# Kernel tuning notes

Hardware: AMD Instinct MI355X
Metric: run time of the kernel (lower is better)

## Reference

```python
import jax, jax.numpy as jnp
import numpy as np

N = 100_000   # nodes
E = 1_600_000 # edges (avg degree 16)
D = 128       # feature dim (input = hidden = output = mlp hidden)
L = 3         # GIN layers
EPS = 0.0     # init_eps, not learned


def setup_inputs() -> dict:
    key = jax.random.key(0)
    ks = jax.random.split(key, 7)
    feat = jax.random.normal(ks[0], (N, D), jnp.float32)
    # scale weights ~ 1/sqrt(fan_in) for numerically sane activations
    W1 = jax.random.normal(ks[1], (L, D, D), jnp.float32) / np.float32(np.sqrt(D))
    b1 = jax.random.normal(ks[2], (L, D), jnp.float32) * 0.01
    W2 = jax.random.normal(ks[3], (L, D, D), jnp.float32) / np.float32(np.sqrt(D))
    b2 = jax.random.normal(ks[4], (L, D), jnp.float32) * 0.01
    src = jax.random.randint(ks[5], (E,), 0, N, dtype=jnp.int32)
    dst = jax.random.randint(ks[6], (E,), 0, N, dtype=jnp.int32)
    return {"feat": feat, "W1": W1, "b1": b1, "W2": W2, "b2": b2,
            "src": src, "dst": dst}


def reference(feat, W1, b1, W2, b2, src, dst):
    h = feat
    for i in range(L):
        # sum-aggregate neighbor (source) features into destination nodes
        neigh = jax.ops.segment_sum(h[src], dst, num_segments=N)  # [N, D]
        rst = (1.0 + EPS) * h + neigh
        # 2-layer MLP: hidden layer uses act+norm(none), last layer is plain linear
        if i < L - 1:
            h1 = jax.nn.relu(rst @ W1[i] + b1[i])
            h2 = h1 @ W2[i] + b2[i]
            h = jax.nn.relu(h2)  # ApplyNodeFunc: norm(none) -> relu
        else:
            # last GIN layer: activation 'none' everywhere
            h1 = rst @ W1[i] + b1[i]
            h = h1 @ W2[i] + b2[i]
    return h
```

## Files before the change

### kernel.cpp

```cpp
#include <hip/hip_runtime.h>
#include <hip/hip_bf16.h>

#define D 128
#define NBUCK_SHIFT 9
#define PAD_SLACK 2048

typedef __bf16 bf16x8 __attribute__((ext_vector_type(8)));
typedef float f32x4 __attribute__((ext_vector_type(4)));
typedef float f32x2 __attribute__((ext_vector_type(2)));
typedef int i32x4 __attribute__((ext_vector_type(4)));
typedef int i32x2 __attribute__((ext_vector_type(2)));
typedef unsigned int u32x4 __attribute__((ext_vector_type(4)));
typedef unsigned short u16x4_t __attribute__((ext_vector_type(4)));
typedef unsigned short u16x8_t __attribute__((ext_vector_type(8)));

__device__ __forceinline__ unsigned short f2b(float f) {
    __hip_bfloat16 h = __float2bfloat16(f);
    return __builtin_bit_cast(unsigned short, h);
}

__device__ __forceinline__ void acc8(f32x2* acc, u32x4 x) {
#pragma unroll
    for (int r = 0; r < 4; ++r) {
        f32x2 t;
        t[0] = __builtin_bit_cast(float, x[r] << 16);
        t[1] = __builtin_bit_cast(float, x[r] & 0xffff0000u);
        acc[r] += t;
    }
}

__global__ __launch_bounds__(256) void coarse_hist_kernel(
        const int* __restrict__ dst, int* __restrict__ bco, int E, int nbuck) {
    __shared__ int s[256];
    int t = threadIdx.x;
    s[t] = 0;
    __syncthreads();
    for (int i = blockIdx.x * 256 + t; i < E; i += gridDim.x * 256)
        atomicAdd(&s[dst[i] >> NBUCK_SHIFT], 1);
    __syncthreads();
    if (t < nbuck && s[t] > 0) atomicAdd(&bco[t], s[t]);
}

__global__ __launch_bounds__(256) void bucket_scan_kernel(
        const int* __restrict__ bco, int* __restrict__ bbase, int nbuck, int E) {
    __shared__ int s[256];
    int t = threadIdx.x;
    int c = (t < nbuck) ? bco[t] : 0;
    s[t] = c;
    __syncthreads();
    for (int o = 1; o < 256; o <<= 1) {
        int y = (t >= o) ? s[t - o] : 0;
        __syncthreads();
        s[t] += y;
        __syncthreads();
    }
    if (t < nbuck) bbase[t] = s[t] - c;
    if (t == 0) bbase[nbuck] = E;
}

__global__ __launch_bounds__(256) void bucket_kernel(
        const int* __restrict__ src, const int* __restrict__ dst,
        const int* __restrict__ bbase, int* __restrict__ bcursor,
        unsigned int* __restrict__ pairs, int E, int nbuck) {
    __shared__ int lcnt[256];
    __shared__ int lbase[256];
    int t = threadIdx.x;
    int base = blockIdx.x * 4096;
    if (t < nbuck) lcnt[t] = 0;
    __syncthreads();
    int d[16], s[16];
#pragma unroll
    for (int k = 0; k < 16; ++k) {
        int i = base + t + k * 256;
        if (i < E) {
            d[k] = dst[i];
            s[k] = src[i];
            atomicAdd(&lcnt[d[k] >> NBUCK_SHIFT], 1);
        } else {
            d[k] = -1;
            s[k] = 0;
        }
    }
    __syncthreads();
    if (t < nbuck) {
        int c = lcnt[t];
        int g = (c > 0) ? atomicAdd(&bcursor[t], c) : 0;
        lbase[t] = bbase[t] + g;
        lcnt[t] = 0;
    }
    __syncthreads();
#pragma unroll
    for (int k = 0; k < 16; ++k) {
        if (d[k] >= 0) {
            int b = d[k] >> NBUCK_SHIFT;
            int r = atomicAdd(&lcnt[b], 1);
            pairs[lbase[b] + r] = ((unsigned)s[k] << 9) | ((unsigned)d[k] & 511u);
        }
    }
}

__global__ __launch_bounds__(1024) void bucket_build_kernel(
        const unsigned int* __restrict__ pairs, const int* __restrict__ bbase,
        i32x2* __restrict__ rowse, int* __restrict__ col, int* __restrict__ rowhead,
        int N, int E) {
    __shared__ int cnt[512];
    __shared__ int off[512];
    int t = threadIdx.x;
    int b = blockIdx.x;
    int s0 = bbase[b], s1 = bbase[b + 1];
    int p0 = ((s0 + 3) & ~3) + b * PAD_SLACK;
    if (t < 512) cnt[t] = 0;
    __syncthreads();
    for (int i = s0 + t; i < s1; i += 1024)
        atomicAdd(&cnt[pairs[i] & 511u], 1);
    __syncthreads();
    int deg = (t < 512) ? cnt[t] : 0;
    int ovp = (deg > 15) ? ((deg - 15 + 3) & ~3) : 0;
    if (t < 512) off[t] = ovp;
    __syncthreads();
    for (int o = 1; o < 512; o <<= 1) {
        int y = (t < 512 && t >= o) ? off[t - o] : 0;
        __syncthreads();
        if (t < 512) off[t] += y;
        __syncthreads();
    }
    int v0 = b << NBUCK_SHIFT;
    int zoff = N << 8;
    if (t < 512) {
        int ex = off[t] - ovp;
        off[t] = ex;
        cnt[t] = 0;
        int v = v0 + t;
        if (v < N) {
            i32x2 se;
            se[0] = p0 + ex;
            se[1] = p0 + ex + ovp;
            rowse[v] = se;
            int* rhv = rowhead + (size_t)v * 16;
            rhv[0] = v << 8;
            int ninl = deg < 15 ? deg : 15;
            for (int q = 1 + ninl; q < 16; ++q) rhv[q] = zoff;
        }
    }
    __syncthreads();
    for (int i = s0 + t; i < s1; i += 1024) {
        unsigned int p = pairs[i];
        int li = (int)(p & 511u);
        int x = (int)(p >> 9);
        int s = atomicAdd(&cnt[li], 1);
        if (s < 15) rowhead[(size_t)(v0 + li) * 16 + 1 + s] = x << 8;
        else        col[p0 + off[li] + (s - 15)] = x << 8;
    }
    __syncthreads();
    if (t < 512) {
        int cc = cnt[t];
        int ovreal = (cc > 15) ? cc - 15 : 0;
        int base2 = p0 + off[t];
        int endp = base2 + ((ovreal + 3) & ~3);
        for (int q = base2 + ovreal; q < endp; ++q) col[q] = zoff;
    }
}

__global__ void f32_to_bf16_kernel(const float4* __restrict__ in, ushort4* __restrict__ out, int n4) {
    int i = blockIdx.x * blockDim.x + threadIdx.x;
    if (i < n4) {
        float4 f = in[i];
        ushort4 o;
        o.x = f2b(f.x); o.y = f2b(f.y); o.z = f2b(f.z); o.w = f2b(f.w);
        out[i] = o;
    }
}

__global__ void wtrans_kernel(const float* __restrict__ W1, const float* __restrict__ W2,
                              unsigned short* __restrict__ W1L, unsigned short* __restrict__ W2L,
                              int total) {
    int i = blockIdx.x * blockDim.x + threadIdx.x;
    if (i < total) {
        int l = i >> 14;
        int rem = i & 16383;
        int k = rem >> 7;
        int n = rem & 127;
        int nt = n >> 4, l15 = n & 15;
        int kb = k >> 5, lg = (k >> 3) & 3, j = k & 7;
        int o = ((l * 32 + nt * 4 + kb) * 64 + lg * 16 + l15) * 8 + j;
        W1L[o] = f2b(W1[i]);
        W2L[o] = f2b(W2[i]);
    }
}

#define RSTRIDE 136
__global__ __launch_bounds__(256, 4) void fused_kernel(
        const unsigned short* __restrict__ h, const i32x2* __restrict__ rowse,
        const int* __restrict__ col, const i32x4* __restrict__ rowhead,
        const unsigned short* __restrict__ W1L, const unsigned short* __restrict__ W2L,
        const float* __restrict__ b1, const float* __restrict__ b2,
        unsigned short* __restrict__ hOut, float* __restrict__ fOut,
        int mode, int ntiles, int N) {
    __shared__ float b1s[128], b2s[128];
    __shared__ unsigned short rstile[16 * RSTRIDE];
    __shared__ unsigned short h1buf[2560];
    int tid = threadIdx.x;
    if (tid < 128) b1s[tid] = b1[tid];
    else b2s[tid - 128] = b2[tid - 128];
    int wave = tid >> 6, lane = tid & 63;
    int v0 = blockIdx.x << 4;

    {
        int i = lane & 15;
        int j = lane >> 4;
        const char* __restrict__ hb = (const char*)h;
        unsigned ioff = (unsigned)i * 16u;
        for (int q = 0; q < 4; ++q) {
            int m = wave * 4 + q;
            int v = v0 + m;
            f32x2 accA[4], accB[4], accC[4], accD[4];
#pragma unroll
            for (int r = 0; r < 4; ++r) {
                accA[r] = (f32x2){0.f, 0.f};
                accB[r] = (f32x2){0.f, 0.f};
                accC[r] = (f32x2){0.f, 0.f};
                accD[r] = (f32x2){0.f, 0.f};
            }
            if (v < N) {
                i32x4 c4 = __builtin_nontemporal_load(&rowhead[(size_t)v * 4 + j]);
                i32x2 se = __builtin_nontemporal_load(&rowse[v]);
                u32x4 x0 = *(const u32x4*)(hb + ((unsigned)c4[0] + ioff));
                u32x4 x1 = *(const u32x4*)(hb + ((unsigned)c4[1] + ioff));
                u32x4 x2 = *(const u32x4*)(hb + ((unsigned)c4[2] + ioff));
                u32x4 x3 = *(const u32x4*)(hb + ((unsigned)c4[3] + ioff));
                int e = se[0] + 4 * j;
                int e1 = se[1];
                bool have = (e < e1);
                i32x4 o4;
                if (have) o4 = __builtin_nontemporal_load((const i32x4*)(col + e));
                acc8(accA, x0);
                acc8(accB, x1);
                acc8(accC, x2);
                acc8(accD, x3);
                while (have) {
                    int en = e + 16;
                    bool haven = (en < e1);
                    i32x4 o4n;
                    if (haven) o4n = __builtin_nontemporal_load((const i32x4*)(col + en));
                    u32x4 y0 = *(const u32x4*)(hb + ((unsigned)o4[0] + ioff));
                    u32x4 y1 = *(const u32x4*)(hb + ((unsigned)o4[1] + ioff));
                    u32x4 y2 = *(const u32x4*)(hb + ((unsigned)o4[2] + ioff));
                    u32x4 y3 = *(const u32x4*)(hb + ((unsigned)o4[3] + ioff));
                    acc8(accA, y0);
                    acc8(accB, y1);
                    acc8(accC, y2);
                    acc8(accD, y3);
                    o4 = o4n;
                    e = en;
                    have = haven;
                }
            }
            unsigned short outv[8];
#pragma unroll
            for (int r = 0; r < 4; ++r) {
                f32x2 s = (accA[r] + accB[r]) + (accC[r] + accD[r]);
                float lo = s[0], hi = s[1];
                lo += __shfl_xor(lo, 16);
                lo += __shfl_xor(lo, 32);
                hi += __shfl_xor(hi, 16);
                hi += __shfl_xor(hi, 32);
                outv[2 * r] = f2b(lo);
                outv[2 * r + 1] = f2b(hi);
            }
            if (j == 0) {
                u16x8_t o;
#pragma unroll
                for (int r = 0; r < 8; ++r) o[r] = outv[r];
                *(u16x8_t*)(rstile + m * RSTRIDE + i * 8) = o;
            }
        }
    }
    __syncthreads();

    int l15 = lane & 15, lg = lane >> 4;
    bf16x8 bfrag[4];
#pragma unroll
    for (int kb = 0; kb < 4; ++kb)
        bfrag[kb] = *(const bf16x8*)(rstile + l15 * RSTRIDE + lg * 8 + kb * 32);

    f32x4 acc[2];
#pragma unroll
    for (int t = 0; t < 2; ++t) acc[t] = (f32x4){0.f, 0.f, 0.f, 0.f};
#pragma unroll
    for (int kb = 0; kb < 4; ++kb)
#pragma unroll
        for (int t = 0; t < 2; ++t) {
            int nt = wave * 2 + t;
            bf16x8 wf = *(const bf16x8*)(W1L + ((nt * 4 + kb) * 64 + lane) * 8);
            acc[t] = __builtin_amdgcn_mfma_f32_16x16x32_bf16(wf, bfrag[kb], acc[t], 0, 0, 0);
        }
#pragma unroll
    for (int t = 0; t < 2; ++t) {
        int nt = wave * 2 + t;
        f32x4 bias = *(const f32x4*)(b1s + nt * 16 + lg * 4);
        int kb2 = nt >> 1;
        int lgk = (nt & 1) * 2 + (lg >> 1);
        int U = kb2 * 80 + l15 * 5 + lgk;
        u16x4_t o;
#pragma unroll
        for (int r = 0; r < 4; ++r) {
            float x = acc[t][r] + bias[r];
            if (mode == 0) x = fmaxf(x, 0.f);
            o[r] = f2b(x);
        }
        *(u16x4_t*)(h1buf + U * 8 + (lg & 1) * 4) = o;
    }
    __syncthreads();
    bf16x8 bf2[4];
#pragma unroll
    for (int kb = 0; kb < 4; ++kb)
        bf2[kb] = *(const bf16x8*)(h1buf + (kb * 80 + l15 * 5 + lg) * 8);
#pragma unroll
    for (int t = 0; t < 2; ++t) acc[t] = (f32x4){0.f, 0.f, 0.f, 0.f};
#pragma unroll
    for (int kb = 0; kb < 4; ++kb)
#pragma unroll
        for (int t = 0; t < 2; ++t) {
            int nt = wave * 2 + t;
            bf16x8 wf = *(const bf16x8*)(W2L + ((nt * 4 + kb) * 64 + lane) * 8);
            acc[t] = __builtin_amdgcn_mfma_f32_16x16x32_bf16(wf, bf2[kb], acc[t], 0, 0, 0);
        }
    int m = v0 + l15;
    if (m < N) {
#pragma unroll
        for (int t = 0; t < 2; ++t) {
            int nt = wave * 2 + t;
            f32x4 bias = *(const f32x4*)(b2s + nt * 16 + lg * 4);
            int c0 = nt * 16 + lg * 4;
            if (mode == 0) {
                u16x4_t o;
#pragma unroll
                for (int r = 0; r < 4; ++r) o[r] = f2b(fmaxf(acc[t][r] + bias[r], 0.f));
                *(u16x4_t*)(hOut + (size_t)m * D + c0) = o;
            } else {
                f32x4 o;
#pragma unroll
                for (int r = 0; r < 4; ++r) o[r] = acc[t][r] + bias[r];
                *(f32x4*)(fOut + (size_t)m * D + c0) = o;
            }
        }
    }
}

extern "C" void kernel_launch(void* const* d_in, const int* in_sizes, int n_in,
                              void* d_out, int out_size, void* d_ws, size_t ws_size,
                              hipStream_t stream) {
    const float* feat = (const float*)d_in[0];
    const float* W1 = (const float*)d_in[1];
    const float* b1 = (const float*)d_in[2];
    const float* W2 = (const float*)d_in[3];
    const float* b2 = (const float*)d_in[4];
    const int* src = (const int*)d_in[5];
    const int* dst = (const int*)d_in[6];

    const int N = in_sizes[0] / D;
    const int L = in_sizes[2] / D;
    const int E = in_sizes[5];

    char* w = (char*)d_ws;
    size_t off = 0;
    auto alloc = [&](size_t bytes) {
        void* p = w + off;
        off = (off + bytes + 255) & ~(size_t)255;
        return p;
    };
    unsigned short* bufA = (unsigned short*)alloc((size_t)(N + 1) * D * 2);
    unsigned short* bufB = (unsigned short*)alloc((size_t)(N + 1) * D * 2);
    unsigned int* pairs = (unsigned int*)alloc((size_t)E * 4);
    int* col = (int*)alloc(((size_t)E + 256 * PAD_SLACK + 16) * 4);
    int* rowhead = (int*)alloc((size_t)N * 16 * 4);
    i32x2* rowse = (i32x2*)alloc((size_t)N * 8);
    int* bco = (int*)alloc(512 * 4);
    int* bcursor = bco + 256;
    int* bbase = (int*)alloc(257 * 4);
    unsigned short* W1L = (unsigned short*)alloc((size_t)L * 16384 * 2);
    unsigned short* W2L = (unsigned short*)alloc((size_t)L * 16384 * 2);

    int nbuck = (N + (1 << NBUCK_SHIFT) - 1) >> NBUCK_SHIFT;

    hipMemsetAsync(bco, 0, 512 * 4, stream);
    hipMemsetAsync(bufA + (size_t)N * D, 0, D * 2, stream);
    hipMemsetAsync(bufB + (size_t)N * D, 0, D * 2, stream);
    coarse_hist_kernel<<<512, 256, 0, stream>>>(dst, bco, E, nbuck);
    bucket_scan_kernel<<<1, 256, 0, stream>>>(bco, bbase, nbuck, E);
    bucket_kernel<<<(E + 4095) / 4096, 256, 0, stream>>>(src, dst, bbase, bcursor, pairs, E, nbuck);
    bucket_build_kernel<<<nbuck, 1024, 0, stream>>>(pairs, bbase, rowse, col, rowhead, N, E);

    int n4 = N * D / 4;
    f32_to_bf16_kernel<<<(n4 + 255) / 256, 256, 0, stream>>>((const float4*)feat, (ushort4*)bufA, n4);
    int wtotal = L * D * D;
    wtrans_kernel<<<(wtotal + 255) / 256, 256, 0, stream>>>(W1, W2, W1L, W2L, wtotal);

    int ntiles = (N + 15) / 16;
    const unsigned short* hin[3] = {bufA, bufB, bufA};
    unsigned short* hout[3] = {bufB, bufA, nullptr};
    for (int i = 0; i < L; ++i) {
        int mode = (i == L - 1) ? 1 : 0;
        fused_kernel<<<ntiles, 256, 0, stream>>>(hin[i], rowse, col, (const i32x4*)rowhead,
                                                 W1L + (size_t)i * 16384, W2L + (size_t)i * 16384,
                                                 b1 + i * D, b2 + i * D, hout[i], (float*)d_out,
                                                 mode, ntiles, N);
    }
}
```

Before: 397.8 us.

## Process two node tiles per 512-thread block with register-resident weight fragments

The fused GIN layer kernel now runs 512-thread blocks that each handle two 16-node tiles. Each of the 8 waves owns one 16-column output slice and loads its W1/W2 fragments into registers once, then reuses them for both tiles. Before, 4 waves each reloaded two slices per tile. This halves the block count and the per-tile global weight loads. The cost is extra VGPR pressure from holding 8 weight vectors per thread, which with launch bounds of 512,4 may cut occupancy or cause spills.

```diff
diff --git a/kernel.cpp b/kernel.cpp
--- a/kernel.cpp
+++ b/kernel.cpp
@@ -189,7 +189,7 @@
 }
 
 #define RSTRIDE 136
-__global__ __launch_bounds__(256, 4) void fused_kernel(
+__global__ __launch_bounds__(512, 4) void fused_kernel(
         const unsigned short* __restrict__ h, const i32x2* __restrict__ rowse,
         const int* __restrict__ col, const i32x4* __restrict__ rowhead,
         const unsigned short* __restrict__ W1L, const unsigned short* __restrict__ W2L,
@@ -197,22 +197,34 @@
         unsigned short* __restrict__ hOut, float* __restrict__ fOut,
         int mode, int ntiles, int N) {
     __shared__ float b1s[128], b2s[128];
-    __shared__ unsigned short rstile[16 * RSTRIDE];
-    __shared__ unsigned short h1buf[2560];
+    __shared__ unsigned short rstile[2][16 * RSTRIDE];
+    __shared__ unsigned short h1buf[2][2560];
     int tid = threadIdx.x;
     if (tid < 128) b1s[tid] = b1[tid];
-    else b2s[tid - 128] = b2[tid - 128];
+    else if (tid < 256) b2s[tid - 128] = b2[tid - 128];
     int wave = tid >> 6, lane = tid & 63;
-    int v0 = blockIdx.x << 4;
+    int l15 = lane & 15, lg = lane >> 4;
+    int tile0 = blockIdx.x * 2;
+
+    u32x4 w1u[4], w2u[4];
+#pragma unroll
+    for (int kb = 0; kb < 4; ++kb) {
+        w1u[kb] = *(const u32x4*)(W1L + ((wave * 4 + kb) * 64 + lane) * 8);
+        w2u[kb] = *(const u32x4*)(W2L + ((wave * 4 + kb) * 64 + lane) * 8);
+    }
+#pragma unroll
+    for (int kb = 0; kb < 4; ++kb)
+        asm volatile("" : "+v"(w1u[kb]), "+v"(w2u[kb]));
+
+    const char* __restrict__ hb = (const char*)h;
 
     {
         int i = lane & 15;
         int j = lane >> 4;
-        const char* __restrict__ hb = (const char*)h;
         unsigned ioff = (unsigned)i * 16u;
         for (int q = 0; q < 4; ++q) {
             int m = wave * 4 + q;
-            int v = v0 + m;
+            int v = (tile0 << 4) + m;
             f32x2 accA[4], accB[4], accC[4], accD[4];
 #pragma unroll
             for (int r = 0; r < 4; ++r) {
@@ -271,77 +283,75 @@
                 u16x8_t o;
 #pragma unroll
                 for (int r = 0; r < 8; ++r) o[r] = outv[r];
-                *(u16x8_t*)(rstile + m * RSTRIDE + i * 8) = o;
-            }
-        }
-    }
-    __syncthreads();
-
-    int l15 = lane & 15, lg = lane >> 4;
-    bf16x8 bfrag[4];
-#pragma unroll
-    for (int kb = 0; kb < 4; ++kb)
-        bfrag[kb] = *(const bf16x8*)(rstile + l15 * RSTRIDE + lg * 8 + kb * 32);
-
-    f32x4 acc[2];
-#pragma unroll
-    for (int t = 0; t < 2; ++t) acc[t] = (f32x4){0.f, 0.f, 0.f, 0.f};
-#pragma unroll
-    for (int kb = 0; kb < 4; ++kb)
-#pragma unroll
-        for (int t = 0; t < 2; ++t) {
-            int nt = wave * 2 + t;
-            bf16x8 wf = *(const bf16x8*)(W1L + ((nt * 4 + kb) * 64 + lane) * 8);
-            acc[t] = __builtin_amdgcn_mfma_f32_16x16x32_bf16(wf, bfrag[kb], acc[t], 0, 0, 0);
-        }
-#pragma unroll
-    for (int t = 0; t < 2; ++t) {
-        int nt = wave * 2 + t;
+                *(u16x8_t*)(rstile[m >> 4] + (m & 15) * RSTRIDE + i * 8) = o;
+            }
+        }
+    }
+    __syncthreads();
+
+    {
+        f32x4 acc[2];
+#pragma unroll
+        for (int t = 0; t < 2; ++t) acc[t] = (f32x4){0.f, 0.f, 0.f, 0.f};
+#pragma unroll
+        for (int kb = 0; kb < 4; ++kb) {
+            bf16x8 wf = __builtin_bit_cast(bf16x8, w1u[kb]);
+#pragma unroll
+            for (int t = 0; t < 2; ++t) {
+                bf16x8 bfrag = *(const bf16x8*)(rstile[t] + l15 * RSTRIDE + lg * 8 + kb * 32);
+                acc[t] = __builtin_amdgcn_mfma_f32_16x16x32_bf16(wf, bfrag, acc[t], 0, 0, 0);
+            }
+        }
+        int nt = wave;
         f32x4 bias = *(const f32x4*)(b1s + nt * 16 + lg * 4);
         int kb2 = nt >> 1;
         int lgk = (nt & 1) * 2 + (lg >> 1);
         int U = kb2 * 80 + l15 * 5 + lgk;
-        u16x4_t o;
-#pragma unroll
-        for (int r = 0; r < 4; ++r) {
-            float x = acc[t][r] + bias[r];
-            if (mode == 0) x = fmaxf(x, 0.f);
-            o[r] = f2b(x);
-        }
-        *(u16x4_t*)(h1buf + U * 8 + (lg & 1) * 4) = o;
-    }
-    __syncthreads();
-    bf16x8 bf2[4];
-#pragma unroll
-    for (int kb = 0; kb < 4; ++kb)
-        bf2[kb] = *(const bf16x8*)(h1buf + (kb * 80 + l15 * 5 + lg) * 8);
-#pragma unroll
-    for (int t = 0; t < 2; ++t) acc[t] = (f32x4){0.f, 0.f, 0.f, 0.f};
-#pragma unroll
-    for (int kb = 0; kb < 4; ++kb)
 #pragma unroll
         for (int t = 0; t < 2; ++t) {
-            int nt = wave * 2 + t;
-            bf16x8 wf = *(const bf16x8*)(W2L + ((nt * 4 + kb) * 64 + lane) * 8);
-            acc[t] = __builtin_amdgcn_mfma_f32_16x16x32_bf16(wf, bf2[kb], acc[t], 0, 0, 0);
-        }
-    int m = v0 + l15;
-    if (m < N) {
+            u16x4_t o;
+#pragma unroll
+            for (int r = 0; r < 4; ++r) {
+                float x = acc[t][r] + bias[r];
+                if (mode == 0) x = fmaxf(x, 0.f);
+                o[r] = f2b(x);
+            }
+            *(u16x4_t*)(h1buf[t] + U * 8 + (lg & 1) * 4) = o;
+        }
+    }
+    __syncthreads();
+
+    {
+        f32x4 acc[2];
+#pragma unroll
+        for (int t = 0; t < 2; ++t) acc[t] = (f32x4){0.f, 0.f, 0.f, 0.f};
+#pragma unroll
+        for (int kb = 0; kb < 4; ++kb) {
+            bf16x8 wf = __builtin_bit_cast(bf16x8, w2u[kb]);
+#pragma unroll
+            for (int t = 0; t < 2; ++t) {
+                bf16x8 bf2 = *(const bf16x8*)(h1buf[t] + (kb * 80 + l15 * 5 + lg) * 8);
+                acc[t] = __builtin_amdgcn_mfma_f32_16x16x32_bf16(wf, bf2, acc[t], 0, 0, 0);
+            }
+        }
+        int nt = wave;
+        f32x4 bias = *(const f32x4*)(b2s + nt * 16 + lg * 4);
+        int c0 = nt * 16 + lg * 4;
 #pragma unroll
         for (int t = 0; t < 2; ++t) {
-            int nt = wave * 2 + t;
-            f32x4 bias = *(const f32x4*)(b2s + nt * 16 + lg * 4);
-            int c0 = nt * 16 + lg * 4;
-            if (mode == 0) {
-                u16x4_t o;
-#pragma unroll
-                for (int r = 0; r < 4; ++r) o[r] = f2b(fmaxf(acc[t][r] + bias[r], 0.f));
-                *(u16x4_t*)(hOut + (size_t)m * D + c0) = o;
-            } else {
-                f32x4 o;
-#pragma unroll
-                for (int r = 0; r < 4; ++r) o[r] = acc[t][r] + bias[r];
-                *(f32x4*)(fOut + (size_t)m * D + c0) = o;
+            int m = ((tile0 + t) << 4) + l15;
+            if (m < N) {
+                if (mode == 0) {
+                    u16x4_t o;
+#pragma unroll
+                    for (int r = 0; r < 4; ++r) o[r] = f2b(fmaxf(acc[t][r] + bias[r], 0.f));
+                    *(u16x4_t*)(hOut + (size_t)m * D + c0) = o;
+                } else {
+                    f32x4 o;
+#pragma unroll
+                    for (int r = 0; r < 4; ++r) o[r] = acc[t][r] + bias[r];
+                    *(f32x4*)(fOut + (size_t)m * D + c0) = o;
+                }
             }
         }
     }
@@ -397,13 +407,14 @@
     wtrans_kernel<<<(wtotal + 255) / 256, 256, 0, stream>>>(W1, W2, W1L, W2L, wtotal);
 
     int ntiles = (N + 15) / 16;
+    int fgrid = (ntiles + 1) / 2;
     const unsigned short* hin[3] = {bufA, bufB, bufA};
     unsigned short* hout[3] = {bufB, bufA, nullptr};
     for (int i = 0; i < L; ++i) {
         int mode = (i == L - 1) ? 1 : 0;
-        fused_kernel<<<ntiles, 256, 0, stream>>>(hin[i], rowse, col, (const i32x4*)rowhead,
-                                                 W1L + (size_t)i * 16384, W2L + (size_t)i * 16384,
-                                                 b1 + i * D, b2 + i * D, hout[i], (float*)d_out,
-                                                 mode, ntiles, N);
-    }
-}
+        fused_kernel<<<fgrid, 512, 0, stream>>>(hin[i], rowse, col, (const i32x4*)rowhead,
+                                                W1L + (size_t)i * 16384, W2L + (size_t)i * 16384,
+                                                b1 + i * D, b2 + i * D, hout[i], (float*)d_out,
+                                                mode, ntiles, N);
+    }
+}
```

Result: slower. 406.8 us (+2.3%).
